# Optimization experiments

Hardware: AMD Instinct MI355X
Metric: run time of the kernel (lower is better)

The kernel has to match this reference:

```python
import jax, jax.numpy as jnp
import numpy as np

D = 64      # node_input_dim == node_hidden_dim
EIN = 16    # edge_input_dim
EH = 64     # edge_hidden_dim
NL, NR = 5000, 15000
EL, ER = 50000, 150000
STEPS = 6
EPS = 1e-5
SLOPE = 0.01


def _ln(x, g, b):
    mu = jnp.mean(x, axis=-1, keepdims=True)
    v = jnp.mean((x - mu) ** 2, axis=-1, keepdims=True)
    return (x - mu) / jnp.sqrt(v + EPS) * g + b


def _lrelu(x):
    return jnp.where(x > 0, x, SLOPE * x)


def setup_inputs() -> dict:
    key = jax.random.key(0)
    ks = jax.random.split(key, 32)

    def n(k, shape, fan_in):
        return jax.random.normal(k, shape, jnp.float32) * (fan_in ** -0.5)

    return {
        'lig_n_feat': jax.random.normal(ks[0], (NL, D), jnp.float32),
        'lig_e_feat': jax.random.normal(ks[1], (EL, EIN), jnp.float32),
        'lig_src': jax.random.randint(ks[2], (EL,), 0, NL),
        'lig_dst': jax.random.randint(ks[3], (EL,), 0, NL),
        'rec_n_feat': jax.random.normal(ks[4], (NR, D), jnp.float32),
        'rec_e_feat': jax.random.normal(ks[5], (ER, EIN), jnp.float32),
        'rec_src': jax.random.randint(ks[6], (ER,), 0, NR),
        'rec_dst': jax.random.randint(ks[7], (ER,), 0, NR),
        'mask': jax.random.uniform(ks[8], (NL, NR), jnp.float32),
        # linear0
        'W0': n(ks[9], (D, D), D), 'b0': jnp.zeros((D,), jnp.float32),
        # edge network: Linear(EIN,EH) -> ReLU -> Linear(EH, D*D)
        'We1': n(ks[10], (EH, EIN), EIN), 'be1': jnp.zeros((EH,), jnp.float32),
        'We2': n(ks[11], (D * D, EH), EH), 'be2': jnp.zeros((D * D,), jnp.float32),
        # NNConv residual fc (no bias) and conv bias
        'resW': n(ks[12], (D, D), D), 'conv_b': jnp.zeros((D,), jnp.float32),
        # message layer Linear(2D, D)
        'msgW': n(ks[13], (D, 2 * D), 2 * D), 'msgb': jnp.zeros((D,), jnp.float32),
        # attention projections (no bias)
        'Qlig': n(ks[14], (D, D), D), 'Klig': n(ks[15], (D, D), D), 'Vlig': n(ks[16], (D, D), D),
        'Qrec': n(ks[17], (D, D), D), 'Krec': n(ks[18], (D, D), D), 'Vrec': n(ks[19], (D, D), D),
        # final LayerNorms
        'g_lig': jnp.ones((D,), jnp.float32), 'b_lig': jnp.zeros((D,), jnp.float32),
        'g_rec': jnp.ones((D,), jnp.float32), 'b_rec': jnp.zeros((D,), jnp.float32),
    }


def _gather_branch(x, efeat, src, dst, n_nodes, W0, b0, We1, be1, We2, be2, resW, conv_b, msgW, msgb):
    # per-edge weight matrices from edge MLP: [E, D, D] (in x out)
    We = jax.nn.relu(efeat @ We1.T + be1) @ We2.T + be2
    We = We.reshape(-1, D, D)
    h = jax.nn.relu(x @ W0.T + b0)
    for _ in range(STEPS):
        msg = jnp.einsum('ei,eio->eo', h[src], We)          # gather + per-edge transform
        agg = jax.ops.segment_sum(msg, dst, num_segments=n_nodes)  # scatter-sum
        m = jax.nn.relu(agg + h @ resW.T + conv_b)           # NNConv residual + bias, relu
        h = jnp.concatenate([m, h], axis=1) @ msgW.T + msgb  # message_layer
    return h + x


def reference(lig_n_feat, lig_e_feat, lig_src, lig_dst, rec_n_feat, rec_e_feat, rec_src, rec_dst,
              mask, W0, b0, We1, be1, We2, be2, resW, conv_b, msgW, msgb,
              Qlig, Klig, Vlig, Qrec, Krec, Vrec, g_lig, b_lig, g_rec, b_rec):
    lig_Fv = _gather_branch(lig_n_feat, lig_e_feat, lig_src, lig_dst, NL,
                            W0, b0, We1, be1, We2, be2, resW, conv_b, msgW, msgb)
    rec_Fv = _gather_branch(rec_n_feat, rec_e_feat, rec_src, rec_dst, NR,
                            W0, b0, We1, be1, We2, be2, resW, conv_b, msgW, msgb)
    hl = _ln(lig_Fv, g_lig, b_lig)
    hr = _ln(rec_Fv, g_rec, b_rec)
    # lig attends to rec
    ql, kr, vr = _lrelu(hl @ Qlig.T), _lrelu(hr @ Krec.T), hr @ Vrec.T
    a = mask * (ql @ kr.T) - 1000.0 * (1.0 - mask)
    att_lig = jax.nn.softmax(a, axis=1) @ vr
    # rec attends to lig
    qr, kl, vl = _lrelu(hr @ Qrec.T), _lrelu(hl @ Klig.T), hl @ Vlig.T
    mt = mask.T
    a2 = mt * (qr @ kl.T) - 1000.0 * (1.0 - mt)
    att_rec = jax.nn.softmax(a2, axis=1) @ vl
    return (_ln(att_lig, g_lig, b_lig), _ln(att_rec, g_rec, b_rec))
```

## Files before the change

### kernel.cpp

```cpp
#include <hip/hip_runtime.h>
#include <hip/hip_bf16.h>

typedef unsigned short ushort_t;
typedef __attribute__((ext_vector_type(8))) short short8_t;
typedef __attribute__((ext_vector_type(4))) float f32x4;
typedef __attribute__((ext_vector_type(4))) unsigned uint4_t;

#define NLIG 5000
#define NREC 15000
#define NTOT 20000
#define ELIG 50000
#define EREC 150000
#define ETOT 200000
#define VSTRIDE 20160
#define NB0 313
#define NB1 938
#define SEGLEN 5000
#define NBA (NB0*3 + NB1)
#define PSLOT 1056

__device__ __forceinline__ float us2f(ushort_t u){
  union { float f; unsigned int i; } x; x.i = ((unsigned int)u) << 16; return x.f;
}
__device__ __forceinline__ ushort_t f2us(float f){
  __hip_bfloat16 b = __float2bfloat16(f);
  return *reinterpret_cast<ushort_t*>(&b);
}
__device__ __forceinline__ unsigned pkbf(float a, float b){
  return (unsigned)f2us(a) | ((unsigned)f2us(b) << 16);
}
__device__ __forceinline__ float wsum64(float v){
#pragma unroll
  for (int s = 32; s >= 1; s >>= 1) v += __shfl_xor(v, s, 64);
  return v;
}
__device__ __forceinline__ f32x4 mfma32(short8_t a, short8_t b, f32x4 c){
  return __builtin_amdgcn_mfma_f32_16x16x32_bf16(a, b, c, 0, 0, 0);
}
__device__ __forceinline__ int geti(const int* __restrict__ p, int i, int i64){
  return i64 ? p[2*i] : p[i];
}

__global__ void kdetect2(const unsigned* __restrict__ xw, const unsigned* __restrict__ iw,
                         int* __restrict__ flagp){
  const int lane = threadIdx.x;
  unsigned w = xw[lane];
  int e0 = (int)((w >> 7) & 0xFF);
  int hit = (e0 >= 100 && e0 <= 134) ? 1 : 0;
  int zodd = ((lane & 1) && iw[lane] == 0u) ? 1 : 0;
#pragma unroll
  for (int s = 32; s >= 1; s >>= 1){
    hit  += __shfl_xor(hit,  s, 64);
    zodd += __shfl_xor(zodd, s, 64);
  }
  if (lane == 0){
    flagp[0] = (hit  >= 40) ? 1 : 0;
    flagp[1] = (zodd >= 24) ? 1 : 0;
  }
}

__global__ void ksent(float* __restrict__ out, int n, float c){
  int i = blockIdx.x*256 + threadIdx.x;
  if (i < n) out[i] = c;
}

__global__ void kcvt_x(const void* __restrict__ lx, const void* __restrict__ rx,
                       const int* __restrict__ flagp, float* __restrict__ xall){
  const int flag = flagp[0];
  const int idx = blockIdx.x*256 + threadIdx.x;
  const void* src; int local;
  if (idx < NLIG*64){ src = lx; local = idx; } else { src = rx; local = idx - NLIG*64; }
  float v;
  if (flag) v = us2f(((const ushort_t*)src)[local]);
  else      v = ((const float*)src)[local];
  xall[idx] = v;
}

struct Srcs { const void* p[20]; };
__global__ void kcvt_w(Srcs S, const int* __restrict__ flagp, float* __restrict__ wcvt){
  const int bounds[21] = {0,4096,4160,5184,5248,267392,271488,275584,275648,283840,
                          283904,288000,292096,296192,300288,304384,308480,308544,308608,308672,308736};
  const int flag = flagp[0];
  const int idx = blockIdx.x*256 + threadIdx.x;
  if (idx >= 308736) return;
  int seg = 0;
#pragma unroll
  for (int s = 1; s < 20; ++s) if (idx >= bounds[s]) seg = s;
  const void* src = S.p[0];
#pragma unroll
  for (int s = 1; s < 20; ++s) if (seg == s) src = S.p[s];
  const int local = idx - bounds[seg];
  float v;
  if (flag) v = us2f(((const ushort_t*)src)[local]);
  else      v = ((const float*)src)[local];
  wcvt[idx] = v;
}

#define W_W0    0
#define W_B0    4096
#define W_WE1   4160
#define W_BE1   5184
#define W_WE2   5248
#define W_BE2   267392
#define W_RESW  271488
#define W_CONVB 275584
#define W_MSGW  275648
#define W_MSGB  283840
#define W_QLIG  283904
#define W_KLIG  288000
#define W_VLIG  292096
#define W_QREC  296192
#define W_KREC  300288
#define W_VREC  304384
#define W_GLIG  308480
#define W_BLIG  308544
#define W_GREC  308608
#define W_BREC  308672

__global__ void kWpk(const float* __restrict__ We2f, ushort_t* __restrict__ Wpk){
  int oidx = blockIdx.x*256 + threadIdx.x;
  int j = oidx & 7, lane = (oidx >> 3) & 63, p = (oidx >> 9) & 1;
  int t = (oidx >> 10) & 3, kb = oidx >> 12;
  int o = t*16 + (lane & 15);
  int gik = kb*32 + (lane >> 4)*8 + j;
  int i = gik >> 6, k = gik & 63;
  float v = We2f[(size_t)(i*64 + o)*64 + k];
  ushort_t hi = f2us(v);
  Wpk[oidx] = p ? f2us(v - us2f(hi)) : hi;
}

__global__ void kh0(const float* __restrict__ xall, const float* __restrict__ W0f,
                    const float* __restrict__ b0f, float* __restrict__ h){
  __shared__ float xr[4][64];
  const int lane = threadIdx.x & 63, wv = threadIdx.x >> 6;
  const int n = blockIdx.x*4 + wv;
  xr[wv][lane] = xall[(size_t)n*64 + lane];
  __syncthreads();
  float acc = b0f[lane];
  const float* wr = W0f + lane*64;
#pragma unroll
  for (int i = 0; i < 64; ++i) acc += xr[wv][i] * wr[i];
  h[(size_t)n*64 + lane] = acc > 0.f ? acc : 0.f;
}

__global__ void khist(const int* __restrict__ ldst, const int* __restrict__ rdst,
                      const int* __restrict__ flagp, int* __restrict__ counts){
  const int i64 = flagp[1];
  const int e = blockIdx.x*256 + threadIdx.x;
  if (e >= ETOT) return;
  int dstg = (e < ELIG) ? geti(ldst, e, i64) : geti(rdst, e - ELIG, i64) + NLIG;
  atomicAdd(&counts[dstg], 1);
}

__global__ __launch_bounds__(1024) void kscan(const int* __restrict__ counts, int* __restrict__ offs){
  __shared__ int part[1024];
  const int tid = threadIdx.x;
  const int PER = 20;
  int loc[PER]; int s = 0;
#pragma unroll
  for (int j = 0; j < PER; ++j){ int idx = tid*PER + j; int v = (idx < NTOT) ? counts[idx] : 0; loc[j] = s; s += v; }
  part[tid] = s;
  __syncthreads();
  for (int d = 1; d < 1024; d <<= 1){
    int add = (tid >= d) ? part[tid - d] : 0;
    __syncthreads();
    part[tid] += add;
    __syncthreads();
  }
  int pre = (tid > 0) ? part[tid - 1] : 0;
#pragma unroll
  for (int j = 0; j < PER; ++j){ int idx = tid*PER + j; if (idx < NTOT) offs[idx] = pre + loc[j]; }
  if (tid == 1023) offs[NTOT] = part[1023];
}

__global__ void kfill(const int* __restrict__ lsrc, const int* __restrict__ ldst,
                      const int* __restrict__ rsrc, const int* __restrict__ rdst,
                      const void* __restrict__ lef, const void* __restrict__ ref_,
                      const int* __restrict__ offs, int* __restrict__ cursor,
                      const int* __restrict__ flagp,
                      int* __restrict__ e_srcn, float* __restrict__ ef_srt){
  const int flag = flagp[0];
  const int i64  = flagp[1];
  const int e = blockIdx.x*256 + threadIdx.x;
  if (e >= ETOT) return;
  int srcg, dstg, le; const void* efb;
  if (e < ELIG){ srcg = geti(lsrc, e, i64); dstg = geti(ldst, e, i64); efb = lef; le = e; }
  else {
    int e2 = e - ELIG;
    srcg = geti(rsrc, e2, i64) + NLIG; dstg = geti(rdst, e2, i64) + NLIG; efb = ref_; le = e2;
  }
  int pos = offs[dstg] + atomicAdd(&cursor[dstg], 1);
  e_srcn[pos] = srcg;
  float* efd = ef_srt + (size_t)pos*16;
  if (flag){
    const ushort_t* efp = (const ushort_t*)efb + (size_t)le*16;
#pragma unroll
    for (int c = 0; c < 16; ++c) efd[c] = us2f(efp[c]);
  } else {
    const float* efp = (const float*)efb + (size_t)le*16;
#pragma unroll
    for (int c = 0; c < 16; ++c) efd[c] = efp[c];
  }
}

__global__ void kz(const float* __restrict__ ef_srt, const float* __restrict__ We1f,
                   const float* __restrict__ be1f, float* __restrict__ z_srt){
  const int lane = threadIdx.x & 63, wv = threadIdx.x >> 6;
  const int e = blockIdx.x*4 + wv;
  const float* efp = ef_srt + (size_t)e*16;
  float acc = be1f[lane];
  const float* wr = We1f + lane*16;
#pragma unroll
  for (int c = 0; c < 16; ++c) acc += efp[c] * wr[c];
  z_srt[(size_t)e*64 + lane] = acc > 0.f ? acc : 0.f;
}

#define SROW 2080
#define SLO  (16*SROW)
__global__ __launch_bounds__(1024)
void kstep(const float* __restrict__ hin, float* __restrict__ hout,
           const int* __restrict__ offs, const int* __restrict__ e_srcn,
           const float* __restrict__ z_srt,
           const ushort_t* __restrict__ Wpk,
           const float* __restrict__ resWf, const float* __restrict__ convbf,
           const float* __restrict__ msgWf, const float* __restrict__ msgbf,
           const float* __restrict__ be2f){
  __shared__ alignas(16) char sbuf[2*SLO];
  __shared__ float h_lds[1024];
  __shared__ float Hs_lds[1024];
  __shared__ float m_lds[1024];
  __shared__ float cbf[64], mbf[64];

  const int tid = threadIdx.x, lane = tid & 63, wv = tid >> 6;
  const int n0 = blockIdx.x * 16;

  h_lds[tid] = hin[(size_t)n0*64 + tid];
  if (tid < 64){ cbf[tid] = convbf[tid]; mbf[tid] = msgbf[tid]; }

  float sacc[64];
#pragma unroll
  for (int i = 0; i < 64; ++i) sacc[i] = 0.f;
  float hs = 0.f;
  {
    const int v = n0 + wv;
    const int jb = offs[v], je = offs[v+1];
    for (int j = jb; j < je; ++j){
      const int sn = e_srcn[j];
      const float zl = z_srt[(size_t)j*64 + lane];
      hs += hin[(size_t)sn*64 + lane];
      const float4* hp = (const float4*)(hin + (size_t)sn*64);
#pragma unroll
      for (int i4 = 0; i4 < 16; ++i4){
        float4 hv = hp[i4];
        sacc[i4*4+0] += hv.x * zl;
        sacc[i4*4+1] += hv.y * zl;
        sacc[i4*4+2] += hv.z * zl;
        sacc[i4*4+3] += hv.w * zl;
      }
    }
    Hs_lds[wv*64 + lane] = hs;
  }

  const int r15 = lane & 15, g4 = lane >> 4;
  const int tW = wv & 3, kq = wv >> 2;
  f32x4 acc; acc[0]=0.f; acc[1]=0.f; acc[2]=0.f; acc[3]=0.f;
#pragma unroll
  for (int c = 0; c < 4; ++c){
#pragma unroll
    for (int ii = 0; ii < 16; ++ii){
      float v = sacc[c*16 + ii];
      ushort_t hi16 = f2us(v);
      unsigned off = (unsigned)(wv*SROW + (ii*64 + lane)*2);
      *(ushort_t*)(sbuf + off) = hi16;
      *(ushort_t*)(sbuf + SLO + off) = f2us(v - us2f(hi16));
    }
    __syncthreads();
    for (int kk = 0; kk < 8; ++kk){
      const int lk = kq*256 + kk*32;
      const int kb = c*32 + kq*8 + kk;
      const unsigned aoff = (unsigned)(r15*SROW + (lk + g4*8)*2);
      const short8_t ah = *(const short8_t*)(sbuf + aoff);
      const short8_t al = *(const short8_t*)(sbuf + SLO + aoff);
      const ushort_t* bp = Wpk + (size_t)(kb*4 + tW)*1024 + lane*8;
      const short8_t bh = *(const short8_t*)(bp);
      const short8_t bl = *(const short8_t*)(bp + 512);
      acc = mfma32(ah, bh, acc);
      acc = mfma32(ah, bl, acc);
      acc = mfma32(al, bh, acc);
    }
    __syncthreads();
  }

  float* redf  = (float*)sbuf;
  float* be2s  = (float*)(sbuf + 16384);
  float* resWt = (float*)(sbuf + 32768);
#pragma unroll
  for (int q = 0; q < 4; ++q)
    redf[kq*1024 + (g4*4 + q)*64 + tW*16 + r15] = acc[q];
  for (int idx = tid; idx < 4096; idx += 1024){
    be2s[idx] = be2f[idx];
    resWt[(idx & 63)*65 + (idx >> 6)] = resWf[idx];
  }
  __syncthreads();
  {
    float aggv = cbf[lane];
#pragma unroll
    for (int k4 = 0; k4 < 4; ++k4) aggv += redf[k4*1024 + wv*64 + lane];
    float t1 = 0.f, t2 = 0.f;
#pragma unroll 8
    for (int i = 0; i < 64; ++i){
      t1 += Hs_lds[wv*64 + i] * be2s[i*64 + lane];
      t2 += h_lds[wv*64 + i]  * resWt[i*65 + lane];
    }
    float mv = aggv + t1 + t2;
    m_lds[wv*64 + lane] = mv > 0.f ? mv : 0.f;
  }
  __syncthreads();
  float* msgWt = (float*)sbuf;
  for (int idx = tid; idx < 8192; idx += 1024)
    msgWt[(idx & 127)*65 + (idx >> 7)] = msgWf[idx];
  __syncthreads();
  {
    float hn = mbf[lane];
#pragma unroll 8
    for (int i = 0; i < 64; ++i){
      hn += m_lds[wv*64 + i] * msgWt[i*65 + lane];
      hn += h_lds[wv*64 + i] * msgWt[(64 + i)*65 + lane];
    }
    hout[(size_t)(n0 + wv)*64 + lane] = hn;
  }
}

__global__ void kfvproj(const float* __restrict__ h, const float* __restrict__ xall,
    const float* __restrict__ wcvt,
    ushort_t* __restrict__ qbh, ushort_t* __restrict__ qbl,
    ushort_t* __restrict__ kbh, ushort_t* __restrict__ kbl,
    ushort_t* __restrict__ vbT){
  __shared__ float hr[4][64];
  const int lane = threadIdx.x & 63, wv = threadIdx.x >> 6;
  const int n = blockIdx.x*4 + wv;
  const bool isLig = n < NLIG;
  const float fv = h[(size_t)n*64 + lane] + xall[(size_t)n*64 + lane];
  const float mu = wsum64(fv) * (1.f/64.f);
  const float dd = fv - mu;
  const float var = wsum64(dd*dd) * (1.f/64.f);
  const float gg = wcvt[(isLig ? W_GLIG : W_GREC) + lane];
  const float bb = wcvt[(isLig ? W_BLIG : W_BREC) + lane];
  const float hl = dd * rsqrtf(var + 1e-5f) * gg + bb;
  hr[wv][lane] = hl;
  __syncthreads();
  const float* Qw = wcvt + (isLig ? W_QLIG : W_QREC) + lane*64;
  const float* Kw = wcvt + (isLig ? W_KLIG : W_KREC) + lane*64;
  const float* Vw = wcvt + (isLig ? W_VLIG : W_VREC) + lane*64;
  float qa = 0.f, ka = 0.f, va = 0.f;
#pragma unroll
  for (int i = 0; i < 64; ++i){
    const float hv = hr[wv][i];
    qa += hv * Qw[i];
    ka += hv * Kw[i];
    va += hv * Vw[i];
  }
  qa = qa > 0.f ? qa : 0.01f*qa;
  ka = ka > 0.f ? ka : 0.01f*ka;
  const size_t o = (size_t)n*64 + lane;
  ushort_t qh = f2us(qa); qbh[o] = qh; qbl[o] = f2us(qa - us2f(qh));
  ushort_t kh = f2us(ka); kbh[o] = kh; kbl[o] = f2us(ka - us2f(kh));
  vbT[(size_t)lane*VSTRIDE + n] = f2us(va);
}

__global__ __launch_bounds__(512)
void kattn3(const ushort_t* __restrict__ qbh, const ushort_t* __restrict__ qbl,
            const ushort_t* __restrict__ kbh, const ushort_t* __restrict__ kbl,
            const ushort_t* __restrict__ vbT, const void* __restrict__ maskp,
            const int* __restrict__ flagp, float* __restrict__ pbuf){
  __shared__ alignas(16) char abuf[34816];
  __shared__ float mred[8][16], lred[8][16];
  float (*m_tile)[16][257] = (float(*)[16][257])abuf;
  float (*ored)[64][17]    = (float(*)[64][17])abuf;

  const int flag = flagp[0];
  const int bx = blockIdx.x;
  const int dirn = (bx < NB0*3) ? 0 : 1;
  const int bid  = dirn ? (bx - NB0*3) : (bx/3);
  const int seg  = dirn ? 0 : (bx - (bx/3)*3);
  const int R   = dirn ? NREC : NLIG;
  const int C   = dirn ? NLIG : NREC;
  const int RNB = dirn ? NLIG : 0;
  const int CNB = dirn ? 0 : NLIG;
  const int cs  = seg * SEGLEN;
  const int ce  = dirn ? C : ((cs + SEGLEN < C) ? cs + SEGLEN : C);

  const int tid = threadIdx.x, lane = tid & 63, wv = tid >> 6;
  const int r15 = lane & 15, g4 = lane >> 4;
  const int rbase = bid * 16;
  int rn = rbase + r15; if (rn > R-1) rn = R-1;

  const ushort_t* qph = qbh + (size_t)(RNB + rn)*64;
  const ushort_t* qpl = qbl + (size_t)(RNB + rn)*64;
  const short8_t qh0a = *(const short8_t*)(qph + g4*8);
  const short8_t qh0b = *(const short8_t*)(qph + 32 + g4*8);
  const short8_t ql0a = *(const short8_t*)(qpl + g4*8);
  const short8_t ql0b = *(const short8_t*)(qpl + 32 + g4*8);

  const int srcA = (((g4 & 1) * 2)     << 4) + r15;
  const int srcB = (((g4 & 1) * 2 + 1) << 4) + r15;
  const bool hiBank = (g4 >> 1) != 0;

  const int s_row = tid >> 5, s_l31 = tid & 31;
  const int s_cl = tid >> 1, s_half = tid & 1;

  float mr[8];
  auto load_tile = [&](int tb2){
    if (dirn == 0){
      int r = rbase + s_row; if (r > R-1) r = R-1;
      const size_t base = (size_t)r*NREC + tb2;
      const int cmax = ce-1 - tb2;
      if (flag){
        const ushort_t* mp = (const ushort_t*)maskp + base;
#pragma unroll
        for (int j = 0; j < 8; ++j){
          int cj = s_l31 + 32*j; if (cj > cmax) cj = cmax;
          mr[j] = us2f(mp[cj]);
        }
      } else {
        const float* mp = (const float*)maskp + base;
#pragma unroll
        for (int j = 0; j < 8; ++j){
          int cj = s_l31 + 32*j; if (cj > cmax) cj = cmax;
          mr[j] = mp[cj];
        }
      }
    } else {
      int c = tb2 + s_cl; if (c > ce-1) c = ce-1;
      int r0 = rbase + s_half*8; if (r0 > R-8) r0 = R-8;
      const size_t base = (size_t)c*NREC + r0;
      if (flag){
        const ushort_t* mp = (const ushort_t*)maskp + base;
        const short8_t v8 = *(const short8_t*)mp;
#pragma unroll
        for (int j = 0; j < 8; ++j) mr[j] = us2f((ushort_t)v8[j]);
      } else {
        const float* mp = (const float*)maskp + base;
        const float4 v0 = *(const float4*)mp;
        const float4 v1 = *(const float4*)(mp + 4);
        mr[0]=v0.x; mr[1]=v0.y; mr[2]=v0.z; mr[3]=v0.w;
        mr[4]=v1.x; mr[5]=v1.y; mr[6]=v1.z; mr[7]=v1.w;
      }
    }
  };

  float mrun = -1e30f, lrun = 0.f;
  f32x4 oacc[4];
#pragma unroll
  for (int t = 0; t < 4; ++t){ oacc[t][0]=0.f; oacc[t][1]=0.f; oacc[t][2]=0.f; oacc[t][3]=0.f; }

  load_tile(cs);
  int buf = 0;
  for (int tb = cs; tb < ce; tb += 256){
    if (dirn == 0){
#pragma unroll
      for (int j = 0; j < 8; ++j) m_tile[buf][s_row][s_l31 + 32*j] = mr[j];
    } else {
#pragma unroll
      for (int j = 0; j < 8; ++j) m_tile[buf][s_half*8 + j][s_cl] = mr[j];
    }
    if (tb + 256 < ce) load_tile(tb + 256);
    __syncthreads();

    const int cb = tb + wv*32;
    int cn0 = cb + r15;      if (cn0 > ce-1) cn0 = ce-1;
    int cn1 = cb + 16 + r15; if (cn1 > ce-1) cn1 = ce-1;
    const ushort_t* kp0h = kbh + (size_t)(CNB + cn0)*64;
    const ushort_t* kp0l = kbl + (size_t)(CNB + cn0)*64;
    const ushort_t* kp1h = kbh + (size_t)(CNB + cn1)*64;
    const ushort_t* kp1l = kbl + (size_t)(CNB + cn1)*64;
    f32x4 st0; st0[0]=0.f; st0[1]=0.f; st0[2]=0.f; st0[3]=0.f;
    f32x4 st1 = st0;
    {
      short8_t ka_ = *(const short8_t*)(kp0h + g4*8);
      short8_t kb_ = *(const short8_t*)(kp0h + 32 + g4*8);
      st0 = mfma32(ka_, qh0a, st0); st0 = mfma32(kb_, qh0b, st0);
      st0 = mfma32(ka_, ql0a, st0); st0 = mfma32(kb_, ql0b, st0);
      short8_t kc_ = *(const short8_t*)(kp0l + g4*8);
      short8_t kd_ = *(const short8_t*)(kp0l + 32 + g4*8);
      st0 = mfma32(kc_, qh0a, st0); st0 = mfma32(kd_, qh0b, st0);
    }
    {
      short8_t ka_ = *(const short8_t*)(kp1h + g4*8);
      short8_t kb_ = *(const short8_t*)(kp1h + 32 + g4*8);
      st1 = mfma32(ka_, qh0a, st1); st1 = mfma32(kb_, qh0b, st1);
      st1 = mfma32(ka_, ql0a, st1); st1 = mfma32(kb_, ql0b, st1);
      short8_t kc_ = *(const short8_t*)(kp1l + g4*8);
      short8_t kd_ = *(const short8_t*)(kp1l + 32 + g4*8);
      st1 = mfma32(kc_, qh0a, st1); st1 = mfma32(kd_, qh0b, st1);
    }
    float sv0[4], sv1[4]; float tmax = -1e30f;
#pragma unroll
    for (int j = 0; j < 4; ++j){
      const int c0 = cb + g4*4 + j, c1 = cb + 16 + g4*4 + j;
      const float mv0 = m_tile[buf][r15][(cb - tb) + g4*4 + j];
      const float mv1 = m_tile[buf][r15][(cb - tb) + 16 + g4*4 + j];
      sv0[j] = (c0 < ce) ? mv0 * (st0[j] + 1000.f) : -1e30f;
      sv1[j] = (c1 < ce) ? mv1 * (st1[j] + 1000.f) : -1e30f;
      tmax = fmaxf(tmax, fmaxf(sv0[j], sv1[j]));
    }
    tmax = fmaxf(tmax, __shfl_xor(tmax, 16, 64));
    tmax = fmaxf(tmax, __shfl_xor(tmax, 32, 64));
    const float mnew = fmaxf(mrun, tmax);
    const float corr = __expf(mrun - mnew);
    float ps0[4], ps1[4], psum = 0.f;
#pragma unroll
    for (int j = 0; j < 4; ++j){
      ps0[j] = __expf(sv0[j] - mnew); psum += ps0[j];
      ps1[j] = __expf(sv1[j] - mnew); psum += ps1[j];
    }
    psum += __shfl_xor(psum, 16, 64);
    psum += __shfl_xor(psum, 32, 64);
    lrun = lrun * corr + psum;
    mrun = mnew;
    const unsigned pk0 = pkbf(ps0[0], ps0[1]);
    const unsigned pk1 = pkbf(ps0[2], ps0[3]);
    const unsigned pk2 = pkbf(ps1[0], ps1[1]);
    const unsigned pk3 = pkbf(ps1[2], ps1[3]);
    const unsigned a0 = (unsigned)__shfl((int)pk0, srcA, 64);
    const unsigned a2 = (unsigned)__shfl((int)pk2, srcA, 64);
    const unsigned a1 = (unsigned)__shfl((int)pk1, srcA, 64);
    const unsigned a3 = (unsigned)__shfl((int)pk3, srcA, 64);
    const unsigned b0 = (unsigned)__shfl((int)pk0, srcB, 64);
    const unsigned b2 = (unsigned)__shfl((int)pk2, srcB, 64);
    const unsigned b1 = (unsigned)__shfl((int)pk1, srcB, 64);
    const unsigned b3 = (unsigned)__shfl((int)pk3, srcB, 64);
    uint4_t pw;
    pw[0] = hiBank ? a2 : a0;
    pw[1] = hiBank ? a3 : a1;
    pw[2] = hiBank ? b2 : b0;
    pw[3] = hiBank ? b3 : b1;
    const short8_t pf8 = *reinterpret_cast<const short8_t*>(&pw);
    const ushort_t* vtb = vbT + (size_t)(CNB + cb + g4*8);
#pragma unroll
    for (int t = 0; t < 4; ++t){
#pragma unroll
      for (int q = 0; q < 4; ++q) oacc[t][q] *= corr;
      const short8_t af = *(const short8_t*)(vtb + (size_t)(t*16 + r15)*VSTRIDE);
      oacc[t] = mfma32(af, pf8, oacc[t]);
    }
    buf ^= 1;
  }

  __syncthreads();
  if (g4 == 0){ mred[wv][r15] = mrun; lred[wv][r15] = lrun; }
#pragma unroll
  for (int t = 0; t < 4; ++t)
#pragma unroll
    for (int q = 0; q < 4; ++q)
      ored[wv][t*16 + g4*4 + q][r15] = oacc[t][q];
  __syncthreads();

  float* ps = pbuf + (size_t)bx * PSLOT;
  for (int rr = 2*wv; rr <= 2*wv + 1; ++rr){
    float mstar = -1e30f;
#pragma unroll
    for (int w = 0; w < 8; ++w) mstar = fmaxf(mstar, mred[w][rr]);
    float lstar = 0.f, ov = 0.f;
#pragma unroll
    for (int w = 0; w < 8; ++w){
      const float e = __expf(mred[w][rr] - mstar);
      lstar += lred[w][rr] * e;
      ov    += ored[w][lane][rr] * e;
    }
    if (lane == 0){ ps[rr] = mstar; ps[16 + rr] = lstar; }
    ps[32 + rr*64 + lane] = ov;
  }
}

__global__ __launch_bounds__(64)
void kcomb(const float* __restrict__ pbuf, const float* __restrict__ wcvt,
           float* __restrict__ out){
  const int rb = blockIdx.x;
  const int lane = threadIdx.x;
  const int dirn = (rb < NB0) ? 0 : 1;
  const int bid  = dirn ? (rb - NB0) : rb;
  const int R    = dirn ? NREC : NLIG;
  const int nseg = dirn ? 1 : 3;
  const int slot0= dirn ? (NB0*3 + bid) : (bid*3);
  const float* gwf = wcvt + (dirn ? W_GREC : W_GLIG);
  const float* bwf = wcvt + (dirn ? W_BREC : W_BLIG);
  float* outp = out + (size_t)(dirn ? NLIG : 0)*64;
  const int rbase = bid * 16;

  for (int rr = 0; rr < 16; ++rr){
    const int rg = rbase + rr;
    if (rg >= R) break;
    float mstar = -1e30f;
    for (int s = 0; s < nseg; ++s)
      mstar = fmaxf(mstar, pbuf[(size_t)(slot0 + s)*PSLOT + rr]);
    float lstar = 0.f, ov = 0.f;
    for (int s = 0; s < nseg; ++s){
      const float* psl = pbuf + (size_t)(slot0 + s)*PSLOT;
      const float e = __expf(psl[rr] - mstar);
      lstar += psl[16 + rr] * e;
      ov    += psl[32 + rr*64 + lane] * e;
    }
    const float att = ov / lstar;
    const float mu = wsum64(att) * (1.f/64.f);
    const float dd = att - mu;
    const float var = wsum64(dd*dd) * (1.f/64.f);
    const float y = dd * rsqrtf(var + 1e-5f) * gwf[lane] + bwf[lane];
    outp[(size_t)rg*64 + lane] = y;
  }
}

extern "C" void kernel_launch(void* const* d_in, const int* in_sizes, int n_in,
                              void* d_out, int out_size, void* d_ws, size_t ws_size,
                              hipStream_t stream){
  const int expsz[29] = {320000,800000,50000,50000,960000,2400000,150000,150000,75000000,
                         4096,64,1024,64,262144,4096,4096,64,8192,64,
                         4096,4096,4096,4096,4096,4096,64,64,64,64};
  bool ok = (n_in == 29);
  if (ok) for (int i = 0; i < 29; ++i) if (in_sizes[i] != expsz[i]) ok = false;
  if (!ok){
    ksent<<<(out_size + 255)/256, 256, 0, stream>>>((float*)d_out, out_size, 10.0f);
    return;
  }

  const void* lig_n = d_in[0];
  const void* lig_e = d_in[1];
  const int* lig_src = (const int*)d_in[2];
  const int* lig_dst = (const int*)d_in[3];
  const void* rec_n = d_in[4];
  const void* rec_e = d_in[5];
  const int* rec_src = (const int*)d_in[6];
  const int* rec_dst = (const int*)d_in[7];
  const void* mask = d_in[8];

  char* p = (char*)d_ws;
  auto carve = [&](size_t bytes)->char*{ char* r = p; p += (bytes + 255) & ~(size_t)255; return r; };
  float*    xall  = (float*)   carve((size_t)NTOT*64*4);
  float*    wcvt  = (float*)   carve((size_t)308736*4);
  float*    h_a   = (float*)   carve((size_t)NTOT*64*4);
  float*    h_b   = (float*)   carve((size_t)NTOT*64*4);
  ushort_t* Wpk   = (ushort_t*)carve((size_t)524288*2);
  ushort_t* qbh   = (ushort_t*)carve((size_t)NTOT*64*2);
  ushort_t* qbl   = (ushort_t*)carve((size_t)NTOT*64*2);
  ushort_t* kbh   = (ushort_t*)carve((size_t)NTOT*64*2);
  ushort_t* kbl   = (ushort_t*)carve((size_t)NTOT*64*2);
  ushort_t* vbT   = (ushort_t*)carve((size_t)64*VSTRIDE*2);
  int*      flag  = (int*)     carve(256);
  int*      counts= (int*)     carve((size_t)2*NTOT*4);
  int*      cursor= counts + NTOT;
  int*      offs  = (int*)     carve((size_t)(NTOT+1)*4);
  int*      e_srcn= (int*)     carve((size_t)ETOT*4);
  float*    ef_srt= (float*)   carve((size_t)ETOT*16*4);
  float*    z_srt = (float*)   carve((size_t)ETOT*64*4);
  float*    pbuf  = ef_srt;

  if ((size_t)(p - (char*)d_ws) > ws_size){
    ksent<<<(out_size + 255)/256, 256, 0, stream>>>((float*)d_out, out_size, 20.0f);
    return;
  }

  Srcs S;
  for (int i = 0; i < 20; ++i) S.p[i] = d_in[9 + i];

  hipMemsetAsync(counts, 0, (size_t)2*NTOT*4, stream);
  hipMemsetAsync(vbT, 0, (size_t)64*VSTRIDE*2, stream);
  kdetect2<<<1, 64, 0, stream>>>((const unsigned*)lig_n, (const unsigned*)lig_src, flag);
  kcvt_x<<<NTOT*64/256, 256, 0, stream>>>(lig_n, rec_n, flag, xall);
  kcvt_w<<<(308736 + 255)/256, 256, 0, stream>>>(S, flag, wcvt);
  kWpk<<<2048, 256, 0, stream>>>(wcvt + W_WE2, Wpk);
  kh0<<<NTOT/4, 256, 0, stream>>>(xall, wcvt + W_W0, wcvt + W_B0, h_a);
  khist<<<(ETOT + 255)/256, 256, 0, stream>>>(lig_dst, rec_dst, flag, counts);
  kscan<<<1, 1024, 0, stream>>>(counts, offs);
  kfill<<<(ETOT + 255)/256, 256, 0, stream>>>(lig_src, lig_dst, rec_src, rec_dst,
                                              lig_e, rec_e, offs, cursor, flag, e_srcn, ef_srt);
  kz<<<ETOT/4, 256, 0, stream>>>(ef_srt, wcvt + W_WE1, wcvt + W_BE1, z_srt);
  float* hi = h_a; float* ho = h_b;
  for (int s = 0; s < 6; ++s){
    kstep<<<NTOT/16, 1024, 0, stream>>>(hi, ho, offs, e_srcn, z_srt, Wpk,
                                        wcvt + W_RESW, wcvt + W_CONVB,
                                        wcvt + W_MSGW, wcvt + W_MSGB, wcvt + W_BE2);
    float* t = hi; hi = ho; ho = t;
  }
  kfvproj<<<NTOT/4, 256, 0, stream>>>(hi, xall, wcvt, qbh, qbl, kbh, kbl, vbT);
  kattn3<<<NBA, 512, 0, stream>>>(qbh, qbl, kbh, kbl, vbT, mask, flag, pbuf);
  kcomb<<<NB0 + NB1, 64, 0, stream>>>(pbuf, wcvt, (float*)d_out);
}
```

Baseline: 2.151 ms.

## Give each attention wave its own row-block and column segment, dropping block barriers

The attention kernel now assigns one independent (row block, column segment) work item per wavefront instead of splitting a block's columns across 8 waves. Mask values are loaded directly into registers (direction 0) or through a per-wave LDS slab (direction 1), so __syncthreads and the in-block cross-wave softmax merge go away. Each wave writes its partial max, sum and output straight to pbuf for the existing combine kernel. The intent is to remove barrier stalls and LDS reduction overhead. The cost is that each wave streams K/V over a much longer column range serially, and the direction-0 mask reads are less coalesced.

```diff
diff --git a/kernel.cpp b/kernel.cpp
--- a/kernel.cpp
+++ b/kernel.cpp
@@ -5,6 +5,7 @@
 typedef __attribute__((ext_vector_type(8))) short short8_t;
 typedef __attribute__((ext_vector_type(4))) float f32x4;
 typedef __attribute__((ext_vector_type(4))) unsigned uint4_t;
+typedef __attribute__((ext_vector_type(2))) unsigned uint2_t;
 
 #define NLIG 5000
 #define NREC 15000
@@ -369,30 +370,28 @@
 }
 
 __global__ __launch_bounds__(512)
-void kattn3(const ushort_t* __restrict__ qbh, const ushort_t* __restrict__ qbl,
+void kattn4(const ushort_t* __restrict__ qbh, const ushort_t* __restrict__ qbl,
             const ushort_t* __restrict__ kbh, const ushort_t* __restrict__ kbl,
             const ushort_t* __restrict__ vbT, const void* __restrict__ maskp,
             const int* __restrict__ flagp, float* __restrict__ pbuf){
-  __shared__ alignas(16) char abuf[34816];
-  __shared__ float mred[8][16], lred[8][16];
-  float (*m_tile)[16][257] = (float(*)[16][257])abuf;
-  float (*ored)[64][17]    = (float(*)[64][17])abuf;
+  __shared__ float slab[8][2][512];
 
   const int flag = flagp[0];
-  const int bx = blockIdx.x;
-  const int dirn = (bx < NB0*3) ? 0 : 1;
-  const int bid  = dirn ? (bx - NB0*3) : (bx/3);
-  const int seg  = dirn ? 0 : (bx - (bx/3)*3);
+  const int tid = threadIdx.x, lane = tid & 63, wv = tid >> 6;
+  const int gw = blockIdx.x*8 + wv;
+  if (gw >= NBA) return;
+  const int dirn = (gw < NB0*3) ? 0 : 1;
+  const int bid  = dirn ? (gw - NB0*3) : (gw/3);
+  const int seg  = dirn ? 0 : (gw - (gw/3)*3);
   const int R   = dirn ? NREC : NLIG;
   const int C   = dirn ? NLIG : NREC;
   const int RNB = dirn ? NLIG : 0;
   const int CNB = dirn ? 0 : NLIG;
-  const int cs  = seg * SEGLEN;
-  const int ce  = dirn ? C : ((cs + SEGLEN < C) ? cs + SEGLEN : C);
-
-  const int tid = threadIdx.x, lane = tid & 63, wv = tid >> 6;
+  const int cs  = dirn ? 0 : seg*SEGLEN;
+  const int ce  = dirn ? C : (cs + SEGLEN);
+
   const int r15 = lane & 15, g4 = lane >> 4;
-  const int rbase = bid * 16;
+  const int rbase = bid*16;
   int rn = rbase + r15; if (rn > R-1) rn = R-1;
 
   const ushort_t* qph = qbh + (size_t)(RNB + rn)*64;
@@ -406,47 +405,44 @@
   const int srcB = (((g4 & 1) * 2 + 1) << 4) + r15;
   const bool hiBank = (g4 >> 1) != 0;
 
-  const int s_row = tid >> 5, s_l31 = tid & 31;
-  const int s_cl = tid >> 1, s_half = tid & 1;
-
-  float mr[8];
-  auto load_tile = [&](int tb2){
-    if (dirn == 0){
-      int r = rbase + s_row; if (r > R-1) r = R-1;
-      const size_t base = (size_t)r*NREC + tb2;
-      const int cmax = ce-1 - tb2;
-      if (flag){
-        const ushort_t* mp = (const ushort_t*)maskp + base;
-#pragma unroll
-        for (int j = 0; j < 8; ++j){
-          int cj = s_l31 + 32*j; if (cj > cmax) cj = cmax;
-          mr[j] = us2f(mp[cj]);
-        }
-      } else {
-        const float* mp = (const float*)maskp + base;
-#pragma unroll
-        for (int j = 0; j < 8; ++j){
-          int cj = s_l31 + 32*j; if (cj > cmax) cj = cmax;
-          mr[j] = mp[cj];
-        }
-      }
+  auto d0_load = [&](int cb, float4 &va, float4 &vb){
+    int cA = cb + g4*4;      if (cA > C-4) cA = C-4;
+    int cB = cb + 16 + g4*4; if (cB > C-4) cB = C-4;
+    if (flag){
+      const ushort_t* mrow = (const ushort_t*)maskp + (size_t)rn*NREC;
+      const uint2_t wa = *(const uint2_t*)(mrow + cA);
+      const uint2_t wb = *(const uint2_t*)(mrow + cB);
+      va.x = us2f((ushort_t)(wa[0] & 0xFFFF)); va.y = us2f((ushort_t)(wa[0] >> 16));
+      va.z = us2f((ushort_t)(wa[1] & 0xFFFF)); va.w = us2f((ushort_t)(wa[1] >> 16));
+      vb.x = us2f((ushort_t)(wb[0] & 0xFFFF)); vb.y = us2f((ushort_t)(wb[0] >> 16));
+      vb.z = us2f((ushort_t)(wb[1] & 0xFFFF)); vb.w = us2f((ushort_t)(wb[1] >> 16));
     } else {
-      int c = tb2 + s_cl; if (c > ce-1) c = ce-1;
-      int r0 = rbase + s_half*8; if (r0 > R-8) r0 = R-8;
-      const size_t base = (size_t)c*NREC + r0;
-      if (flag){
-        const ushort_t* mp = (const ushort_t*)maskp + base;
-        const short8_t v8 = *(const short8_t*)mp;
-#pragma unroll
-        for (int j = 0; j < 8; ++j) mr[j] = us2f((ushort_t)v8[j]);
-      } else {
-        const float* mp = (const float*)maskp + base;
-        const float4 v0 = *(const float4*)mp;
-        const float4 v1 = *(const float4*)(mp + 4);
-        mr[0]=v0.x; mr[1]=v0.y; mr[2]=v0.z; mr[3]=v0.w;
-        mr[4]=v1.x; mr[5]=v1.y; mr[6]=v1.z; mr[7]=v1.w;
-      }
-    }
+      const float* mrow = (const float*)maskp + (size_t)rn*NREC;
+      va = *(const float4*)(mrow + cA);
+      vb = *(const float4*)(mrow + cB);
+    }
+  };
+  const int s_c = lane >> 1, s_h = lane & 1;
+  auto d1_load = [&](int cb, float4 &va, float4 &vb){
+    int c = cb + s_c; if (c > C-1) c = C-1;
+    int r0 = rbase + s_h*8; if (r0 > R-8) r0 = R-8;
+    const size_t base = (size_t)c*NREC + r0;
+    if (flag){
+      const ushort_t* mp = (const ushort_t*)maskp + base;
+      const short8_t v8 = *(const short8_t*)mp;
+      va.x = us2f((ushort_t)v8[0]); va.y = us2f((ushort_t)v8[1]);
+      va.z = us2f((ushort_t)v8[2]); va.w = us2f((ushort_t)v8[3]);
+      vb.x = us2f((ushort_t)v8[4]); vb.y = us2f((ushort_t)v8[5]);
+      vb.z = us2f((ushort_t)v8[6]); vb.w = us2f((ushort_t)v8[7]);
+    } else {
+      const float* mp = (const float*)maskp + base;
+      va = *(const float4*)mp;
+      vb = *(const float4*)(mp + 4);
+    }
+  };
+  auto d1_write = [&](int b, const float4 &va, const float4 &vb){
+    float* s = &slab[wv][b][s_c*16 + s_h*8];
+    *(float4*)s = va; *(float4*)(s + 4) = vb;
   };
 
   float mrun = -1e30f, lrun = 0.f;
@@ -454,22 +450,33 @@
 #pragma unroll
   for (int t = 0; t < 4; ++t){ oacc[t][0]=0.f; oacc[t][1]=0.f; oacc[t][2]=0.f; oacc[t][3]=0.f; }
 
-  load_tile(cs);
+  float4 pA, pB;
+  if (dirn == 0) d0_load(cs, pA, pB);
+  else { d1_load(cs, pA, pB); d1_write(0, pA, pB); d1_load(cs + 32, pA, pB); }
+
   int buf = 0;
-  for (int tb = cs; tb < ce; tb += 256){
+  for (int cb = cs; cb < ce; cb += 32){
+    float mv0[4], mv1[4];
     if (dirn == 0){
-#pragma unroll
-      for (int j = 0; j < 8; ++j) m_tile[buf][s_row][s_l31 + 32*j] = mr[j];
+      mv0[0]=pA.x; mv0[1]=pA.y; mv0[2]=pA.z; mv0[3]=pA.w;
+      mv1[0]=pB.x; mv1[1]=pB.y; mv1[2]=pB.z; mv1[3]=pB.w;
+      if (cb + 32 < ce) d0_load(cb + 32, pA, pB);
     } else {
-#pragma unroll
-      for (int j = 0; j < 8; ++j) m_tile[buf][s_half*8 + j][s_cl] = mr[j];
-    }
-    if (tb + 256 < ce) load_tile(tb + 256);
-    __syncthreads();
-
-    const int cb = tb + wv*32;
-    int cn0 = cb + r15;      if (cn0 > ce-1) cn0 = ce-1;
-    int cn1 = cb + 16 + r15; if (cn1 > ce-1) cn1 = ce-1;
+      const float* s = &slab[wv][buf][0];
+#pragma unroll
+      for (int j = 0; j < 4; ++j){
+        mv0[j] = s[(g4*4 + j)*16 + r15];
+        mv1[j] = s[(16 + g4*4 + j)*16 + r15];
+      }
+      if (cb + 32 < ce){
+        d1_write(buf ^ 1, pA, pB);
+        if (cb + 64 < ce) d1_load(cb + 64, pA, pB);
+      }
+      buf ^= 1;
+    }
+
+    int cn0 = cb + r15;      if (cn0 > C-1) cn0 = C-1;
+    int cn1 = cb + 16 + r15; if (cn1 > C-1) cn1 = C-1;
     const ushort_t* kp0h = kbh + (size_t)(CNB + cn0)*64;
     const ushort_t* kp0l = kbl + (size_t)(CNB + cn0)*64;
     const ushort_t* kp1h = kbh + (size_t)(CNB + cn1)*64;
@@ -498,10 +505,8 @@
 #pragma unroll
     for (int j = 0; j < 4; ++j){
       const int c0 = cb + g4*4 + j, c1 = cb + 16 + g4*4 + j;
-      const float mv0 = m_tile[buf][r15][(cb - tb) + g4*4 + j];
-      const float mv1 = m_tile[buf][r15][(cb - tb) + 16 + g4*4 + j];
-      sv0[j] = (c0 < ce) ? mv0 * (st0[j] + 1000.f) : -1e30f;
-      sv1[j] = (c1 < ce) ? mv1 * (st1[j] + 1000.f) : -1e30f;
+      sv0[j] = (c0 < ce) ? mv0[j] * (st0[j] + 1000.f) : -1e30f;
+      sv1[j] = (c1 < ce) ? mv1[j] * (st1[j] + 1000.f) : -1e30f;
       tmax = fmaxf(tmax, fmaxf(sv0[j], sv1[j]));
     }
     tmax = fmaxf(tmax, __shfl_xor(tmax, 16, 64));
@@ -544,33 +549,15 @@
       const short8_t af = *(const short8_t*)(vtb + (size_t)(t*16 + r15)*VSTRIDE);
       oacc[t] = mfma32(af, pf8, oacc[t]);
     }
-    buf ^= 1;
-  }
-
-  __syncthreads();
-  if (g4 == 0){ mred[wv][r15] = mrun; lred[wv][r15] = lrun; }
+  }
+
+  float* ps = pbuf + (size_t)gw * PSLOT;
+  if (g4 == 0){ ps[r15] = mrun; ps[16 + r15] = lrun; }
 #pragma unroll
   for (int t = 0; t < 4; ++t)
 #pragma unroll
     for (int q = 0; q < 4; ++q)
-      ored[wv][t*16 + g4*4 + q][r15] = oacc[t][q];
-  __syncthreads();
-
-  float* ps = pbuf + (size_t)bx * PSLOT;
-  for (int rr = 2*wv; rr <= 2*wv + 1; ++rr){
-    float mstar = -1e30f;
-#pragma unroll
-    for (int w = 0; w < 8; ++w) mstar = fmaxf(mstar, mred[w][rr]);
-    float lstar = 0.f, ov = 0.f;
-#pragma unroll
-    for (int w = 0; w < 8; ++w){
-      const float e = __expf(mred[w][rr] - mstar);
-      lstar += lred[w][rr] * e;
-      ov    += ored[w][lane][rr] * e;
-    }
-    if (lane == 0){ ps[rr] = mstar; ps[16 + rr] = lstar; }
-    ps[32 + rr*64 + lane] = ov;
-  }
+      ps[32 + r15*64 + t*16 + g4*4 + q] = oacc[t][q];
 }
 
 __global__ __launch_bounds__(64)
@@ -682,6 +669,6 @@
     float* t = hi; hi = ho; ho = t;
   }
   kfvproj<<<NTOT/4, 256, 0, stream>>>(hi, xall, wcvt, qbh, qbl, kbh, kbl, vbT);
-  kattn3<<<NBA, 512, 0, stream>>>(qbh, qbl, kbh, kbl, vbT, mask, flag, pbuf);
+  kattn4<<<(NBA + 7)/8, 512, 0, stream>>>(qbh, qbl, kbh, kbl, vbT, mask, flag, pbuf);
   kcomb<<<NB0 + NB1, 64, 0, stream>>>(pbuf, wcvt, (float*)d_out);
 }
```

After: 2.153 ms. About the same (+0.1%).
